# Kernel tuning notes

Measured on AMD Instinct MI355X. Metric: run time of the kernel, lower is better.

The kernel has to match this reference:

```python
import jax, jax.numpy as jnp
import numpy as np

GRID = 480  # grid extent for both x and y voxel indices


def setup_inputs() -> dict:
    key = jax.random.key(0)
    k = jax.random.split(key, 8)
    B, N, FD, H1, H2, D = 4, 100000, 3, 128, 256, 64
    scale = 0.05
    pt_fea = jax.random.normal(k[0], (B, N, FD), dtype=jnp.float32)
    xy_ind = jax.random.randint(k[1], (B, N, 2), 0, GRID, dtype=jnp.int32)
    W1 = jax.random.normal(k[2], (FD, H1), dtype=jnp.float32) * scale
    b1 = jnp.zeros((H1,), dtype=jnp.float32)
    W2 = jax.random.normal(k[3], (H1, H2), dtype=jnp.float32) * scale
    b2 = jnp.zeros((H2,), dtype=jnp.float32)
    W3 = jax.random.normal(k[4], (H2, D), dtype=jnp.float32) * scale
    b3 = jnp.zeros((D,), dtype=jnp.float32)
    return {"pt_fea": pt_fea, "xy_ind": xy_ind, "W1": W1, "b1": b1,
            "W2": W2, "b2": b2, "W3": W3, "b3": b3}


def reference(pt_fea, xy_ind, W1, b1, W2, b2, W3, b3):
    B, N, FD = pt_fea.shape
    flat = pt_fea.reshape(B * N, FD)
    # pad xy_ind with batch id -> (b, x, y) per point
    bidx = jnp.repeat(jnp.arange(B, dtype=xy_ind.dtype), N)
    xy = xy_ind.reshape(B * N, 2)
    # lexicographic linear encoding so sorted linear order == torch.unique(dim=0) row order
    lin = (bidx.astype(jnp.int32) * GRID + xy[:, 0]) * GRID + xy[:, 1]
    unq_lin, unq_inv = jnp.unique(lin, return_inverse=True)
    M = int(unq_lin.shape[0])  # concrete: indices are concrete (eager unique)
    unq = jnp.stack([unq_lin // (GRID * GRID),
                     (unq_lin // GRID) % GRID,
                     unq_lin % GRID], axis=1)
    # per-point MLP: 3 -> 128 -> 256 -> 64
    h = jax.nn.relu(flat @ W1 + b1)
    h = jax.nn.relu(h @ W2 + b2)
    feat = h @ W3 + b3
    # scatter_max pooling per unique voxel
    pooled = jax.ops.segment_max(feat, unq_inv.reshape(-1), num_segments=M)
    return unq, pooled
```

## Files before the change

### kernel.cpp

```cpp
#include <hip/hip_runtime.h>
#include <hip/hip_bf16.h>

#define GRIDW 480
#define CELLS_PER_B (GRIDW*GRIDW)
#define NCELL (4*CELLS_PER_B)
#define NPTS  400000
#define NPB   100000
#define H1D 128
#define H2D 256
#define DD 64
#define SCAN_BLK 900
#define NTILE 6250
#define GRIDP 512
#define NSUB  25000
#define CNT_NB 1563
#define EMIT_NB 3600

typedef unsigned short u16;
typedef __attribute__((ext_vector_type(8))) short bf16x8;
typedef __attribute__((ext_vector_type(4))) float f32x4;
typedef __attribute__((ext_vector_type(4))) unsigned u32x4;
typedef __attribute__((ext_vector_type(2))) unsigned u32x2;

static __device__ __forceinline__ u16 f2bf(float f){
  unsigned u = __float_as_uint(f);
  unsigned r = u + 0x7FFFu + ((u>>16)&1u);
  return (u16)(r>>16);
}
static __device__ __forceinline__ float bf2f(u16 b){
  return __uint_as_float(((unsigned)b) << 16);
}
static __device__ __forceinline__ unsigned cvt_pk_bf16(float lo, float hi){
  unsigned r;
  asm("v_cvt_pk_bf16_f32 %0, %1, %2" : "=v"(r) : "v"(lo), "v"(hi));
  return r;
}

static __device__ __forceinline__ void pack_one(int e, const float* W2, const float* W3,
                                                u16* bp2, u16* bp3){
  if (e < 32768){
    int j = e & 7, c = (e>>3)&15, ko = (e>>7)&15, n = e>>11;
    bp2[e] = f2bf(W2[(ko*8+j)*H2D + n*16 + c]);
  } else {
    int e3 = e - 32768;
    int j = e3 & 7, c = (e3>>3)&15, ko = (e3>>7)&31, n = e3>>12;
    bp3[e3] = f2bf(W3[(ko*8+j)*DD + n*16 + c]);
  }
}

__global__ void k_countpack(const int* __restrict__ xy, unsigned* __restrict__ counts,
                            const float* __restrict__ W2, const float* __restrict__ W3,
                            u16* __restrict__ bp2, u16* __restrict__ bp3){
  int b = blockIdx.x;
  if (b < CNT_NB){
    int p = b*256 + threadIdx.x;
    if (p < NPTS){
      int bb = p / NPB;
      int x = xy[2*p], y = xy[2*p+1];
      atomicAdd(&counts[(bb*GRIDW + x)*GRIDW + y], 1u);
    }
  } else {
    int e = (b - CNT_NB)*256 + threadIdx.x;
    if (e < 49152) pack_one(e, W2, W3, bp2, bp3);
  }
}

__global__ void k_scan2(const unsigned* __restrict__ counts,
                        unsigned* __restrict__ rankF, unsigned* __restrict__ rankC,
                        unsigned* __restrict__ bsumF, unsigned* __restrict__ bsumC){
  __shared__ unsigned shF[256], shC[256];
  int tid = threadIdx.x;
  int base = blockIdx.x*1024 + tid*4;
  unsigned c0=counts[base], c1=counts[base+1], c2=counts[base+2], c3=counts[base+3];
  unsigned f0=c0?1u:0u, f1=c1?1u:0u, f2=c2?1u:0u, f3=c3?1u:0u;
  unsigned sF=f0+f1+f2+f3, sC=c0+c1+c2+c3;
  shF[tid]=sF; shC[tid]=sC; __syncthreads();
  for (int off=1; off<256; off<<=1){
    unsigned tF = (tid>=off) ? shF[tid-off] : 0u;
    unsigned tC = (tid>=off) ? shC[tid-off] : 0u;
    __syncthreads();
    shF[tid] += tF; shC[tid] += tC;
    __syncthreads();
  }
  unsigned eF = shF[tid]-sF, eC = shC[tid]-sC;
  if (tid==255){ bsumF[blockIdx.x]=shF[255]; bsumC[blockIdx.x]=shC[255]; }
  rankF[base]=eF; rankF[base+1]=eF+f0; rankF[base+2]=eF+f0+f1; rankF[base+3]=eF+f0+f1+f2;
  rankC[base]=eC; rankC[base+1]=eC+c0; rankC[base+2]=eC+c0+c1; rankC[base+3]=eC+c0+c1+c2;
}

__global__ void k_scan_bsum2(unsigned* __restrict__ bsumF, unsigned* __restrict__ bsumC){
  __shared__ unsigned shF[1024], shC[1024];
  int tid = threadIdx.x;
  unsigned vF = (tid<SCAN_BLK) ? bsumF[tid] : 0u;
  unsigned vC = (tid<SCAN_BLK) ? bsumC[tid] : 0u;
  shF[tid]=vF; shC[tid]=vC; __syncthreads();
  for (int off=1; off<1024; off<<=1){
    unsigned tF = (tid>=off) ? shF[tid-off] : 0u;
    unsigned tC = (tid>=off) ? shC[tid-off] : 0u;
    __syncthreads();
    shF[tid] += tF; shC[tid] += tC;
    __syncthreads();
  }
  if (tid<SCAN_BLK){ bsumF[tid]=shF[tid]-vF; bsumC[tid]=shC[tid]-vC; }
}

__global__ void k_emitscatter(
    const unsigned* __restrict__ counts,
    const unsigned* __restrict__ rankF, unsigned* __restrict__ rankC,
    const unsigned* __restrict__ bsumF, const unsigned* __restrict__ bsumC,
    const int* __restrict__ xy,
    unsigned* __restrict__ perm, unsigned* __restrict__ vox,
    float* __restrict__ out){
  int b = blockIdx.x;
  if (b < EMIT_NB){
    int i = b*256 + threadIdx.x;
    if (counts[i]){
      unsigned rF = rankF[i] + bsumF[i>>10];
      int bb = i / CELLS_PER_B;
      int rem = i - bb*CELLS_PER_B;
      int x = rem / GRIDW;
      int y = rem - x*GRIDW;
      float* o = out + 3u*rF;
      o[0]=(float)bb; o[1]=(float)x; o[2]=(float)y;
    }
  } else {
    int p = (b - EMIT_NB)*256 + threadIdx.x;
    if (p < NPTS){
      int bb = p / NPB;
      int x = xy[2*p], y = xy[2*p+1];
      int cell = (bb*GRIDW+x)*GRIDW + y;
      unsigned slot = atomicAdd(&rankC[cell], 1u) + bsumC[cell>>10];
      perm[slot] = (unsigned)p;
      vox[slot]  = rankF[cell] + bsumF[cell>>10];
    }
  }
}

__global__ __launch_bounds__(256,2) void k_mlpp(
    const float* __restrict__ pt, const unsigned* __restrict__ perm,
    const unsigned* __restrict__ vox,
    const u16* __restrict__ bp2, const u16* __restrict__ bp3,
    const float* __restrict__ W1, const float* __restrict__ b1,
    const float* __restrict__ b2, const float* __restrict__ b3,
    float* __restrict__ outp,
    unsigned* __restrict__ pvf, unsigned* __restrict__ pvl,
    u16* __restrict__ pmf, u16* __restrict__ pml)
{
  __shared__ __attribute__((aligned(16))) u16 h1s[64*128];
  __shared__ __attribute__((aligned(16))) u16 h2s[2][64*64];
  __shared__ __attribute__((aligned(16))) u16 w3s[16384];
  __shared__ __attribute__((aligned(16))) float cf[832];
  __shared__ __attribute__((aligned(16))) float in_s[192];
  __shared__ unsigned vox_s[64];

  const int tid  = threadIdx.x;
  const int lane = tid & 63;
  const int w    = tid >> 6;
  const int g    = lane >> 4;
  const int p    = lane & 15;
  const int wn   = w & 1;
  const int wp   = w >> 1;
  const int oct  = tid & 15;

  for (int i = tid; i < 2048; i += 256)
    *(u32x4*)((char*)w3s + i*16) = *(const u32x4*)((const char*)bp3 + i*16);
  for (int i = tid; i < 832; i += 256){
    float v;
    if (i < 384) v = W1[i];
    else if (i < 512) v = b1[i-384];
    else if (i < 768) v = b2[i-512];
    else v = b3[i-768];
    cf[i] = v;
  }

  bf16x8 wf2[32];
  #pragma unroll
  for (int c=0;c<4;++c)
    #pragma unroll
    for (int nn=0;nn<2;++nn)
      #pragma unroll
      for (int t=0;t<4;++t){
        int ngl = c*4 + 2*wn + nn;
        wf2[(c*2+nn)*4+t] = *(const bf16x8*)(bp2 + (((ngl*16 + t*4 + g)*16) + p)*8);
      }

  int tile = blockIdx.x;
  unsigned pmN = 0;
  float pf0=0.f, pf1=0.f, pf2=0.f;
  if (tid < 64){
    unsigned pm0 = perm[(size_t)tile*64 + tid];
    const float* q = pt + 3*(size_t)pm0;
    pf0 = q[0]; pf1 = q[1]; pf2 = q[2];
    if (tile + GRIDP < NTILE) pmN = perm[(size_t)(tile+GRIDP)*64 + tid];
  }
  __syncthreads();

  for (; tile < NTILE; tile += GRIDP){
    if (tid < 64){ in_s[tid*3]=pf0; in_s[tid*3+1]=pf1; in_s[tid*3+2]=pf2; }
    unsigned vr = 0;
    if (tid < 64) vr = vox[(size_t)tile*64 + tid];
    __syncthreads();
    if (tid < 64 && tile + GRIDP < NTILE){
      const float* q = pt + 3*(size_t)pmN;
      pf0 = q[0]; pf1 = q[1]; pf2 = q[2];
    }
    unsigned pmN2 = 0;
    if (tid < 64 && tile + 2*GRIDP < NTILE)
      pmN2 = perm[(size_t)(tile+2*GRIDP)*64 + tid];

    {
      f32x4 w1v[3][2], b1v[2];
      #pragma unroll
      for (int f=0;f<3;++f){
        w1v[f][0] = *(const f32x4*)&cf[f*128 + oct*8];
        w1v[f][1] = *(const f32x4*)&cf[f*128 + oct*8 + 4];
      }
      b1v[0] = *(const f32x4*)&cf[384 + oct*8];
      b1v[1] = *(const f32x4*)&cf[384 + oct*8 + 4];
      #pragma unroll
      for (int q=0;q<4;++q){
        int row = q*16 + (tid>>4);
        float x0 = in_s[row*3+0], x1 = in_s[row*3+1], x2 = in_s[row*3+2];
        f32x4 a0 = b1v[0], a1 = b1v[1];
        #pragma unroll
        for (int i=0;i<4;++i){
          a0[i] = fmaf(x0, w1v[0][0][i], a0[i]);
          a1[i] = fmaf(x0, w1v[0][1][i], a1[i]);
          a0[i] = fmaf(x1, w1v[1][0][i], a0[i]);
          a1[i] = fmaf(x1, w1v[1][1][i], a1[i]);
          a0[i] = fmaf(x2, w1v[2][0][i], a0[i]);
          a1[i] = fmaf(x2, w1v[2][1][i], a1[i]);
          a0[i] = fmaxf(a0[i], 0.f);
          a1[i] = fmaxf(a1[i], 0.f);
        }
        u32x4 ov;
        ov[0] = cvt_pk_bf16(a0[0], a0[1]);
        ov[1] = cvt_pk_bf16(a0[2], a0[3]);
        ov[2] = cvt_pk_bf16(a1[0], a1[1]);
        ov[3] = cvt_pk_bf16(a1[2], a1[3]);
        unsigned byte = ((unsigned)row<<8) + (unsigned)oct*16u;
        byte ^= (unsigned)(row&7) << 4;
        *(u32x4*)((char*)h1s + byte) = ov;
      }
    }
    if (tid < 64) vox_s[tid] = vr;
    __syncthreads();

    bf16x8 hf[2][4];
    #pragma unroll
    for (int pp=0;pp<2;++pp){
      int row = (2*wp+pp)*16 + p;
      #pragma unroll
      for (int t=0;t<4;++t){
        unsigned byte = ((unsigned)row<<8) + (unsigned)t*64u + (unsigned)g*16u;
        byte ^= (unsigned)(row&7) << 4;
        hf[pp][t] = *(const bf16x8*)((const char*)h1s + byte);
      }
    }

    f32x4 acc3[2][2];
    #pragma unroll
    for (int a=0;a<2;++a)
      #pragma unroll
      for (int b=0;b<2;++b){ acc3[a][b][0]=0.f; acc3[a][b][1]=0.f; acc3[a][b][2]=0.f; acc3[a][b][3]=0.f; }

    #pragma unroll
    for (int c=0;c<4;++c){
      f32x4 acc2[2][2];
      #pragma unroll
      for (int a=0;a<2;++a)
        #pragma unroll
        for (int b=0;b<2;++b){ acc2[a][b][0]=0.f; acc2[a][b][1]=0.f; acc2[a][b][2]=0.f; acc2[a][b][3]=0.f; }
      #pragma unroll
      for (int t=0;t<4;++t)
        #pragma unroll
        for (int nn=0;nn<2;++nn)
          #pragma unroll
          for (int pp=0;pp<2;++pp)
            acc2[nn][pp] = __builtin_amdgcn_mfma_f32_16x16x32_bf16(
                wf2[(c*2+nn)*4+t], hf[pp][t], acc2[nn][pp], 0, 0, 0);
      u16* h2 = h2s[c & 1];
      #pragma unroll
      for (int nn=0;nn<2;++nn){
        f32x4 b2v = *(const f32x4*)&cf[512 + c*64 + (2*wn+nn)*16 + g*4];
        #pragma unroll
        for (int pp=0;pp<2;++pp){
          int point = (2*wp+pp)*16 + p;
          float e0 = fmaxf(acc2[nn][pp][0] + b2v[0], 0.f);
          float e1 = fmaxf(acc2[nn][pp][1] + b2v[1], 0.f);
          float e2 = fmaxf(acc2[nn][pp][2] + b2v[2], 0.f);
          float e3 = fmaxf(acc2[nn][pp][3] + b2v[3], 0.f);
          u32x2 o2; o2[0] = cvt_pk_bf16(e0, e1); o2[1] = cvt_pk_bf16(e2, e3);
          unsigned byte = (unsigned)point*128u + (unsigned)((2*wn+nn)*32 + g*8);
          byte ^= (unsigned)(point&7) << 4;
          *(u32x2*)((char*)h2 + byte) = o2;
        }
      }
      __syncthreads();
      #pragma unroll
      for (int t2=0;t2<2;++t2){
        bf16x8 w3f[2], h2f[2];
        #pragma unroll
        for (int dn=0;dn<2;++dn){
          int dt = 2*wn + dn;
          unsigned wb = (unsigned)(((dt*32 + (c*2+t2)*4 + g)*16 + p)*16);
          w3f[dn] = *(const bf16x8*)((const char*)w3s + wb);
        }
        #pragma unroll
        for (int pp=0;pp<2;++pp){
          int point = (2*wp+pp)*16 + p;
          unsigned byte = (unsigned)point*128u + (unsigned)t2*64u + (unsigned)g*16u;
          byte ^= (unsigned)(point&7) << 4;
          h2f[pp] = *(const bf16x8*)((const char*)h2 + byte);
        }
        #pragma unroll
        for (int dn=0;dn<2;++dn)
          #pragma unroll
          for (int pp=0;pp<2;++pp)
            acc3[dn][pp] = __builtin_amdgcn_mfma_f32_16x16x32_bf16(
                w3f[dn], h2f[pp], acc3[dn][pp], 0, 0, 0);
      }
    }

    #pragma unroll
    for (int dn=0;dn<2;++dn){
      f32x4 b3v = *(const f32x4*)&cf[768 + (2*wn+dn)*16 + g*4];
      #pragma unroll
      for (int pp=0;pp<2;++pp){
        int point = (2*wp+pp)*16 + p;
        float e0 = acc3[dn][pp][0] + b3v[0];
        float e1 = acc3[dn][pp][1] + b3v[1];
        float e2 = acc3[dn][pp][2] + b3v[2];
        float e3 = acc3[dn][pp][3] + b3v[3];
        u32x2 o2; o2[0] = cvt_pk_bf16(e0, e1); o2[1] = cvt_pk_bf16(e2, e3);
        unsigned byte = (unsigned)point*128u + (unsigned)((2*wn+dn)*32 + g*8);
        byte ^= (unsigned)(point&7) << 4;
        *(u32x2*)((char*)h2s[0] + byte) = o2;
      }
    }
    __syncthreads();

    {
      int st = tile*4 + w;
      float val[16]; unsigned vid[16];
      #pragma unroll
      for (int r=0;r<16;++r){
        int row = w*16 + r;
        unsigned byte = (unsigned)row*128u + (unsigned)lane*2u;
        byte ^= (unsigned)(row&7) << 4;
        val[r] = bf2f(*(const u16*)((const char*)h2s[0] + byte));
        vid[r] = vox_s[row];
      }
      float m = val[0];
      unsigned vprev = vid[0];
      int runstart = 0;
      #pragma unroll
      for (int r=1;r<16;++r){
        if (vid[r] != vprev){
          if (runstart == 0){
            pmf[(size_t)st*64 + lane] = (u16)(__float_as_uint(m)>>16);
            if (lane==0) pvf[st] = vprev;
          } else {
            outp[(size_t)vprev*64 + lane] = m;
          }
          m = val[r]; runstart = r; vprev = vid[r];
        } else m = fmaxf(m, val[r]);
      }
      pml[(size_t)st*64 + lane] = (u16)(__float_as_uint(m)>>16);
      if (lane==0) pvl[st] = vprev;
      if (runstart == 0){
        pmf[(size_t)st*64 + lane] = (u16)(__float_as_uint(m)>>16);
        if (lane==0) pvf[st] = vprev;
      }
    }
    __syncthreads();
    pmN = pmN2;
  }
}

__global__ __launch_bounds__(256) void k_fixup(
    const unsigned* __restrict__ pvf, const unsigned* __restrict__ pvl,
    const u16* __restrict__ pmf, const u16* __restrict__ pml,
    float* __restrict__ outp){
  int t  = blockIdx.x*4 + (threadIdx.x>>6);
  int ch = threadIdx.x & 63;
  if (t >= NSUB) return;
  unsigned vf = pvf[t], vl = pvl[t];
  if (t == 0 || pvl[t-1] != vf){
    float m = bf2f(pmf[(size_t)t*64 + ch]);
    if (vl == vf){
      m = fmaxf(m, bf2f(pml[(size_t)t*64 + ch]));
      int k = t+1;
      while (k < NSUB && pvf[k] == vf){
        m = fmaxf(m, bf2f(pmf[(size_t)k*64 + ch]));
        if (pvl[k] != vf) break;
        m = fmaxf(m, bf2f(pml[(size_t)k*64 + ch]));
        ++k;
      }
    }
    outp[(size_t)vf*64 + ch] = m;
  }
  if (vl != vf){
    float m = bf2f(pml[(size_t)t*64 + ch]);
    int k = t+1;
    while (k < NSUB && pvf[k] == vl){
      m = fmaxf(m, bf2f(pmf[(size_t)k*64 + ch]));
      if (pvl[k] != vl) break;
      m = fmaxf(m, bf2f(pml[(size_t)k*64 + ch]));
      ++k;
    }
    outp[(size_t)vl*64 + ch] = m;
  }
}

extern "C" void kernel_launch(void* const* d_in, const int* in_sizes, int n_in,
                              void* d_out, int out_size, void* d_ws, size_t ws_size,
                              hipStream_t stream){
  const float* pt = (const float*)d_in[0];
  const int*   xy = (const int*)d_in[1];
  const float* W1 = (const float*)d_in[2];
  const float* b1 = (const float*)d_in[3];
  const float* W2 = (const float*)d_in[4];
  const float* b2 = (const float*)d_in[5];
  const float* W3 = (const float*)d_in[6];
  const float* b3 = (const float*)d_in[7];
  float* out = (float*)d_out;

  int M = out_size / 67;
  float* outp = out + 3*(size_t)M;

  unsigned* counts = (unsigned*)d_ws;
  unsigned* rankF  = counts + NCELL;
  unsigned* rankC  = rankF + NCELL;
  unsigned* bsumF  = rankC + NCELL;
  unsigned* bsumC  = bsumF + 1024;
  unsigned* perm   = bsumC + 1024;
  unsigned* vox    = perm + NPTS;
  unsigned* pvf    = vox + NPTS;
  unsigned* pvl    = pvf + NSUB;
  u16* bp2 = (u16*)(pvl + NSUB);
  u16* bp3 = bp2 + 32768;
  u16* pmf = bp3 + 16384;
  u16* pml = pmf + (size_t)NSUB*64;

  hipMemsetAsync(counts, 0, NCELL*sizeof(unsigned), stream);
  k_countpack  <<<CNT_NB+192, 256, 0, stream>>>(xy, counts, W2, W3, bp2, bp3);
  k_scan2      <<<SCAN_BLK, 256, 0, stream>>>(counts, rankF, rankC, bsumF, bsumC);
  k_scan_bsum2 <<<1, 1024, 0, stream>>>(bsumF, bsumC);
  k_emitscatter<<<EMIT_NB+CNT_NB, 256, 0, stream>>>(counts, rankF, rankC, bsumF, bsumC,
                                                    xy, perm, vox, out);
  k_mlpp       <<<GRIDP, 256, 0, stream>>>(pt, perm, vox, bp2, bp3, W1, b1, b2, b3,
                                           outp, pvf, pvl, pmf, pml);
  k_fixup      <<<NSUB/4, 256, 0, stream>>>(pvf, pvl, pmf, pml, outp);
}
```

Baseline: 152.6 us.

## Make MLP kernel wave-independent with per-wave 16-point tiles and no block barriers

Restructures the fused MLP+pooling kernel so each wave processes its own 16-point subtile end to end. Layer 1 is computed directly into MFMA B-fragments in registers via shuffles instead of through shared memory. W2 now lives in LDS and W3 is read from global/cache instead of the reverse. Each wave uses a private LDS buffer for h2 and the output, which removes all __syncthreads in the main loop. The cost is that W2 fragments are re-read from LDS every subtile instead of kept in registers, and W3 is read from global memory in the inner loop.

```diff
diff --git a/kernel.cpp b/kernel.cpp
--- a/kernel.cpp
+++ b/kernel.cpp
@@ -10,9 +10,9 @@
 #define H2D 256
 #define DD 64
 #define SCAN_BLK 900
-#define NTILE 6250
 #define GRIDP 512
 #define NSUB  25000
+#define NWAVES (GRIDP*4)
 #define CNT_NB 1563
 #define EMIT_NB 3600
 
@@ -146,24 +146,18 @@
     unsigned* __restrict__ pvf, unsigned* __restrict__ pvl,
     u16* __restrict__ pmf, u16* __restrict__ pml)
 {
-  __shared__ __attribute__((aligned(16))) u16 h1s[64*128];
-  __shared__ __attribute__((aligned(16))) u16 h2s[2][64*64];
-  __shared__ __attribute__((aligned(16))) u16 w3s[16384];
+  __shared__ __attribute__((aligned(16))) u16 w2s[32768];
   __shared__ __attribute__((aligned(16))) float cf[832];
-  __shared__ __attribute__((aligned(16))) float in_s[192];
-  __shared__ unsigned vox_s[64];
+  __shared__ __attribute__((aligned(16))) u16 h2p[4][1024];
 
   const int tid  = threadIdx.x;
   const int lane = tid & 63;
   const int w    = tid >> 6;
   const int g    = lane >> 4;
   const int p    = lane & 15;
-  const int wn   = w & 1;
-  const int wp   = w >> 1;
-  const int oct  = tid & 15;
-
-  for (int i = tid; i < 2048; i += 256)
-    *(u32x4*)((char*)w3s + i*16) = *(const u32x4*)((const char*)bp3 + i*16);
+
+  for (int i = tid; i < 4096; i += 256)
+    *(u32x4*)((char*)w2s + i*16) = *(const u32x4*)((const char*)bp2 + i*16);
   for (int i = tid; i < 832; i += 256){
     float v;
     if (i < 384) v = W1[i];
@@ -172,184 +166,132 @@
     else v = b3[i-768];
     cf[i] = v;
   }
-
-  bf16x8 wf2[32];
-  #pragma unroll
-  for (int c=0;c<4;++c)
-    #pragma unroll
-    for (int nn=0;nn<2;++nn)
-      #pragma unroll
-      for (int t=0;t<4;++t){
-        int ngl = c*4 + 2*wn + nn;
-        wf2[(c*2+nn)*4+t] = *(const bf16x8*)(bp2 + (((ngl*16 + t*4 + g)*16) + p)*8);
-      }
-
-  int tile = blockIdx.x;
-  unsigned pmN = 0;
-  float pf0=0.f, pf1=0.f, pf2=0.f;
-  if (tid < 64){
-    unsigned pm0 = perm[(size_t)tile*64 + tid];
+  __syncthreads();
+
+  u16* hb = h2p[w];
+
+  const int wid = blockIdx.x*4 + w;
+  int st = wid;
+
+  float pf0=0.f, pf1=0.f, pf2=0.f; unsigned vx=0, pmN=0;
+  if (lane < 16 && st < NSUB){
+    unsigned pm0 = perm[(size_t)st*16 + lane];
     const float* q = pt + 3*(size_t)pm0;
     pf0 = q[0]; pf1 = q[1]; pf2 = q[2];
-    if (tile + GRIDP < NTILE) pmN = perm[(size_t)(tile+GRIDP)*64 + tid];
-  }
-  __syncthreads();
-
-  for (; tile < NTILE; tile += GRIDP){
-    if (tid < 64){ in_s[tid*3]=pf0; in_s[tid*3+1]=pf1; in_s[tid*3+2]=pf2; }
-    unsigned vr = 0;
-    if (tid < 64) vr = vox[(size_t)tile*64 + tid];
-    __syncthreads();
-    if (tid < 64 && tile + GRIDP < NTILE){
+    vx = vox[(size_t)st*16 + lane];
+    if (st + NWAVES < NSUB) pmN = perm[(size_t)(st+NWAVES)*16 + lane];
+  }
+
+  for (; st < NSUB; st += NWAVES){
+    float nf0=0.f, nf1=0.f, nf2=0.f; unsigned nvx=0, pmN2=0;
+    if (lane < 16 && st + NWAVES < NSUB){
       const float* q = pt + 3*(size_t)pmN;
-      pf0 = q[0]; pf1 = q[1]; pf2 = q[2];
-    }
-    unsigned pmN2 = 0;
-    if (tid < 64 && tile + 2*GRIDP < NTILE)
-      pmN2 = perm[(size_t)(tile+2*GRIDP)*64 + tid];
-
-    {
-      f32x4 w1v[3][2], b1v[2];
-      #pragma unroll
-      for (int f=0;f<3;++f){
-        w1v[f][0] = *(const f32x4*)&cf[f*128 + oct*8];
-        w1v[f][1] = *(const f32x4*)&cf[f*128 + oct*8 + 4];
-      }
-      b1v[0] = *(const f32x4*)&cf[384 + oct*8];
-      b1v[1] = *(const f32x4*)&cf[384 + oct*8 + 4];
-      #pragma unroll
-      for (int q=0;q<4;++q){
-        int row = q*16 + (tid>>4);
-        float x0 = in_s[row*3+0], x1 = in_s[row*3+1], x2 = in_s[row*3+2];
-        f32x4 a0 = b1v[0], a1 = b1v[1];
-        #pragma unroll
-        for (int i=0;i<4;++i){
-          a0[i] = fmaf(x0, w1v[0][0][i], a0[i]);
-          a1[i] = fmaf(x0, w1v[0][1][i], a1[i]);
-          a0[i] = fmaf(x1, w1v[1][0][i], a0[i]);
-          a1[i] = fmaf(x1, w1v[1][1][i], a1[i]);
-          a0[i] = fmaf(x2, w1v[2][0][i], a0[i]);
-          a1[i] = fmaf(x2, w1v[2][1][i], a1[i]);
-          a0[i] = fmaxf(a0[i], 0.f);
-          a1[i] = fmaxf(a1[i], 0.f);
-        }
-        u32x4 ov;
-        ov[0] = cvt_pk_bf16(a0[0], a0[1]);
-        ov[1] = cvt_pk_bf16(a0[2], a0[3]);
-        ov[2] = cvt_pk_bf16(a1[0], a1[1]);
-        ov[3] = cvt_pk_bf16(a1[2], a1[3]);
-        unsigned byte = ((unsigned)row<<8) + (unsigned)oct*16u;
-        byte ^= (unsigned)(row&7) << 4;
-        *(u32x4*)((char*)h1s + byte) = ov;
-      }
-    }
-    if (tid < 64) vox_s[tid] = vr;
-    __syncthreads();
-
-    bf16x8 hf[2][4];
+      nf0 = q[0]; nf1 = q[1]; nf2 = q[2];
+      nvx = vox[(size_t)(st+NWAVES)*16 + lane];
+      if (st + 2*NWAVES < NSUB) pmN2 = perm[(size_t)(st+2*NWAVES)*16 + lane];
+    }
+
+    float x0 = __shfl(pf0, p, 64);
+    float x1 = __shfl(pf1, p, 64);
+    float x2 = __shfl(pf2, p, 64);
+
+    bf16x8 hf[4];
     #pragma unroll
-    for (int pp=0;pp<2;++pp){
-      int row = (2*wp+pp)*16 + p;
-      #pragma unroll
-      for (int t=0;t<4;++t){
-        unsigned byte = ((unsigned)row<<8) + (unsigned)t*64u + (unsigned)g*16u;
-        byte ^= (unsigned)(row&7) << 4;
-        hf[pp][t] = *(const bf16x8*)((const char*)h1s + byte);
-      }
-    }
-
-    f32x4 acc3[2][2];
+    for (int t=0;t<4;++t){
+      int cb = t*32 + g*8;
+      f32x4 wa0 = *(const f32x4*)&cf[cb];
+      f32x4 wa1 = *(const f32x4*)&cf[cb+4];
+      f32x4 wb0 = *(const f32x4*)&cf[128+cb];
+      f32x4 wb1 = *(const f32x4*)&cf[128+cb+4];
+      f32x4 wc0 = *(const f32x4*)&cf[256+cb];
+      f32x4 wc1 = *(const f32x4*)&cf[256+cb+4];
+      f32x4 a0  = *(const f32x4*)&cf[384+cb];
+      f32x4 a1  = *(const f32x4*)&cf[384+cb+4];
+      #pragma unroll
+      for (int i=0;i<4;++i){
+        a0[i] = fmaf(x0, wa0[i], a0[i]);
+        a1[i] = fmaf(x0, wa1[i], a1[i]);
+        a0[i] = fmaf(x1, wb0[i], a0[i]);
+        a1[i] = fmaf(x1, wb1[i], a1[i]);
+        a0[i] = fmaf(x2, wc0[i], a0[i]);
+        a1[i] = fmaf(x2, wc1[i], a1[i]);
+        a0[i] = fmaxf(a0[i], 0.f);
+        a1[i] = fmaxf(a1[i], 0.f);
+      }
+      u32x4 ov;
+      ov[0] = cvt_pk_bf16(a0[0], a0[1]);
+      ov[1] = cvt_pk_bf16(a0[2], a0[3]);
+      ov[2] = cvt_pk_bf16(a1[0], a1[1]);
+      ov[3] = cvt_pk_bf16(a1[2], a1[3]);
+      hf[t] = *(bf16x8*)&ov;
+    }
+
+    f32x4 acc3[4];
     #pragma unroll
-    for (int a=0;a<2;++a)
-      #pragma unroll
-      for (int b=0;b<2;++b){ acc3[a][b][0]=0.f; acc3[a][b][1]=0.f; acc3[a][b][2]=0.f; acc3[a][b][3]=0.f; }
+    for (int a=0;a<4;++a){ acc3[a][0]=0.f; acc3[a][1]=0.f; acc3[a][2]=0.f; acc3[a][3]=0.f; }
 
     #pragma unroll
     for (int c=0;c<4;++c){
-      f32x4 acc2[2][2];
-      #pragma unroll
-      for (int a=0;a<2;++a)
+      f32x4 acc2[4];
+      #pragma unroll
+      for (int a=0;a<4;++a){ acc2[a][0]=0.f; acc2[a][1]=0.f; acc2[a][2]=0.f; acc2[a][3]=0.f; }
+      #pragma unroll
+      for (int t=0;t<4;++t){
         #pragma unroll
-        for (int b=0;b<2;++b){ acc2[a][b][0]=0.f; acc2[a][b][1]=0.f; acc2[a][b][2]=0.f; acc2[a][b][3]=0.f; }
-      #pragma unroll
-      for (int t=0;t<4;++t)
+        for (int nn=0;nn<4;++nn){
+          int ngl = c*4 + nn;
+          bf16x8 w2f = *(const bf16x8*)((const char*)w2s +
+                          (((ngl*16 + t*4 + g)*16) + p)*16);
+          acc2[nn] = __builtin_amdgcn_mfma_f32_16x16x32_bf16(w2f, hf[t], acc2[nn], 0, 0, 0);
+        }
+      }
+      #pragma unroll
+      for (int nn=0;nn<4;++nn){
+        f32x4 b2v = *(const f32x4*)&cf[512 + c*64 + nn*16 + g*4];
+        float e0 = fmaxf(acc2[nn][0] + b2v[0], 0.f);
+        float e1 = fmaxf(acc2[nn][1] + b2v[1], 0.f);
+        float e2 = fmaxf(acc2[nn][2] + b2v[2], 0.f);
+        float e3 = fmaxf(acc2[nn][3] + b2v[3], 0.f);
+        u32x2 o2; o2[0] = cvt_pk_bf16(e0, e1); o2[1] = cvt_pk_bf16(e2, e3);
+        unsigned byte = (unsigned)p*128u + (unsigned)(nn*32 + g*8);
+        byte ^= (unsigned)(p&7) << 4;
+        *(u32x2*)((char*)hb + byte) = o2;
+      }
+      #pragma unroll
+      for (int t2=0;t2<2;++t2){
+        int s = c*2 + t2;
+        unsigned hbyte = (unsigned)p*128u + (unsigned)(t2*64 + g*16);
+        hbyte ^= (unsigned)(p&7) << 4;
+        bf16x8 h2f = *(const bf16x8*)((const char*)hb + hbyte);
         #pragma unroll
-        for (int nn=0;nn<2;++nn)
-          #pragma unroll
-          for (int pp=0;pp<2;++pp)
-            acc2[nn][pp] = __builtin_amdgcn_mfma_f32_16x16x32_bf16(
-                wf2[(c*2+nn)*4+t], hf[pp][t], acc2[nn][pp], 0, 0, 0);
-      u16* h2 = h2s[c & 1];
-      #pragma unroll
-      for (int nn=0;nn<2;++nn){
-        f32x4 b2v = *(const f32x4*)&cf[512 + c*64 + (2*wn+nn)*16 + g*4];
-        #pragma unroll
-        for (int pp=0;pp<2;++pp){
-          int point = (2*wp+pp)*16 + p;
-          float e0 = fmaxf(acc2[nn][pp][0] + b2v[0], 0.f);
-          float e1 = fmaxf(acc2[nn][pp][1] + b2v[1], 0.f);
-          float e2 = fmaxf(acc2[nn][pp][2] + b2v[2], 0.f);
-          float e3 = fmaxf(acc2[nn][pp][3] + b2v[3], 0.f);
-          u32x2 o2; o2[0] = cvt_pk_bf16(e0, e1); o2[1] = cvt_pk_bf16(e2, e3);
-          unsigned byte = (unsigned)point*128u + (unsigned)((2*wn+nn)*32 + g*8);
-          byte ^= (unsigned)(point&7) << 4;
-          *(u32x2*)((char*)h2 + byte) = o2;
+        for (int dt=0;dt<4;++dt){
+          bf16x8 w3f = *(const bf16x8*)(bp3 + (((dt*32 + s*4 + g)*16) + p)*8);
+          acc3[dt] = __builtin_amdgcn_mfma_f32_16x16x32_bf16(w3f, h2f, acc3[dt], 0, 0, 0);
         }
       }
-      __syncthreads();
-      #pragma unroll
-      for (int t2=0;t2<2;++t2){
-        bf16x8 w3f[2], h2f[2];
-        #pragma unroll
-        for (int dn=0;dn<2;++dn){
-          int dt = 2*wn + dn;
-          unsigned wb = (unsigned)(((dt*32 + (c*2+t2)*4 + g)*16 + p)*16);
-          w3f[dn] = *(const bf16x8*)((const char*)w3s + wb);
-        }
-        #pragma unroll
-        for (int pp=0;pp<2;++pp){
-          int point = (2*wp+pp)*16 + p;
-          unsigned byte = (unsigned)point*128u + (unsigned)t2*64u + (unsigned)g*16u;
-          byte ^= (unsigned)(point&7) << 4;
-          h2f[pp] = *(const bf16x8*)((const char*)h2 + byte);
-        }
-        #pragma unroll
-        for (int dn=0;dn<2;++dn)
-          #pragma unroll
-          for (int pp=0;pp<2;++pp)
-            acc3[dn][pp] = __builtin_amdgcn_mfma_f32_16x16x32_bf16(
-                w3f[dn], h2f[pp], acc3[dn][pp], 0, 0, 0);
-      }
     }
 
     #pragma unroll
-    for (int dn=0;dn<2;++dn){
-      f32x4 b3v = *(const f32x4*)&cf[768 + (2*wn+dn)*16 + g*4];
-      #pragma unroll
-      for (int pp=0;pp<2;++pp){
-        int point = (2*wp+pp)*16 + p;
-        float e0 = acc3[dn][pp][0] + b3v[0];
-        float e1 = acc3[dn][pp][1] + b3v[1];
-        float e2 = acc3[dn][pp][2] + b3v[2];
-        float e3 = acc3[dn][pp][3] + b3v[3];
-        u32x2 o2; o2[0] = cvt_pk_bf16(e0, e1); o2[1] = cvt_pk_bf16(e2, e3);
-        unsigned byte = (unsigned)point*128u + (unsigned)((2*wn+dn)*32 + g*8);
-        byte ^= (unsigned)(point&7) << 4;
-        *(u32x2*)((char*)h2s[0] + byte) = o2;
-      }
-    }
-    __syncthreads();
+    for (int dt=0;dt<4;++dt){
+      f32x4 b3v = *(const f32x4*)&cf[768 + dt*16 + g*4];
+      float e0 = acc3[dt][0] + b3v[0];
+      float e1 = acc3[dt][1] + b3v[1];
+      float e2 = acc3[dt][2] + b3v[2];
+      float e3 = acc3[dt][3] + b3v[3];
+      u32x2 o2; o2[0] = cvt_pk_bf16(e0, e1); o2[1] = cvt_pk_bf16(e2, e3);
+      unsigned byte = (unsigned)p*128u + (unsigned)(dt*32 + g*8);
+      byte ^= (unsigned)(p&7) << 4;
+      *(u32x2*)((char*)hb + byte) = o2;
+    }
 
     {
-      int st = tile*4 + w;
       float val[16]; unsigned vid[16];
       #pragma unroll
       for (int r=0;r<16;++r){
-        int row = w*16 + r;
-        unsigned byte = (unsigned)row*128u + (unsigned)lane*2u;
-        byte ^= (unsigned)(row&7) << 4;
-        val[r] = bf2f(*(const u16*)((const char*)h2s[0] + byte));
-        vid[r] = vox_s[row];
+        unsigned byte = (unsigned)r*128u + (unsigned)lane*2u;
+        byte ^= (unsigned)(r&7) << 4;
+        val[r] = bf2f(*(const u16*)((const char*)hb + byte));
+        vid[r] = __shfl(vx, r, 64);
       }
       float m = val[0];
       unsigned vprev = vid[0];
@@ -373,8 +315,7 @@
         if (lane==0) pvf[st] = vprev;
       }
     }
-    __syncthreads();
-    pmN = pmN2;
+    pf0=nf0; pf1=nf1; pf2=nf2; vx=nvx; pmN=pmN2;
   }
 }
 
```

Result: faster. 145.5 us (median of 3 runs) (-4.6%).
